# Performance work log

Hardware: AMD Instinct MI355X
Metric: run time of the kernel (lower is better)

Reference implementation:

```python
import jax, jax.numpy as jnp
import numpy as np
from jax import lax

STRIDE = (1, 1)
PADDING = ((1, 1), (1, 1))


@jax.custom_vjp
def ternary_quantize(w):
    """Quantize OIHW weights to {-1,0,+1} with per-output-channel scale alpha."""
    abs_w = jnp.abs(w)
    delta = 0.7 * abs_w.mean(axis=(1, 2, 3), keepdims=True)          # [O,1,1,1]
    ternary = jnp.where(w > delta, 1.0, jnp.where(w < -delta, -1.0, 0.0)).astype(w.dtype)
    mask = ternary != 0
    count = jnp.maximum(mask.sum(axis=(1, 2, 3), keepdims=True), 1).astype(w.dtype)
    alpha = (abs_w * mask.astype(w.dtype)).sum(axis=(1, 2, 3), keepdims=True) / count
    return ternary, alpha


def _tq_fwd(w):
    return ternary_quantize(w), w


def _tq_bwd(w, grads):
    g_ternary, _g_alpha = grads  # STE: grad_alpha is discarded
    g = jnp.where(jnp.abs(w) > 1.0, 0.0, g_ternary)
    return (g,)


ternary_quantize.defvjp(_tq_fwd, _tq_bwd)


def setup_inputs() -> dict:
    key = jax.random.key(0)
    kx, kw = jax.random.split(key)
    x = jax.random.normal(kx, (32, 256, 56, 56), dtype=jnp.float32)
    # kaiming_normal fan_out: std = sqrt(2 / (out_ch * kH * kW))
    std = np.sqrt(2.0 / (256 * 3 * 3)).astype(np.float32)
    weight = jax.random.normal(kw, (256, 256, 3, 3), dtype=jnp.float32) * std
    return {"x": x, "weight": weight}


def reference(x, weight):
    ternary, alpha = ternary_quantize(weight)
    scaled_w = alpha * ternary  # values in {-alpha_o, 0, +alpha_o}
    return lax.conv_general_dilated(
        x, scaled_w,
        window_strides=STRIDE,
        padding=PADDING,
        dimension_numbers=("NCHW", "OIHW", "NCHW"),
    )
```

## Files before the change

### kernel.cpp

```cpp
#include <hip/hip_runtime.h>
#include <hip/hip_bf16.h>

typedef unsigned short u16;
typedef __bf16 bf16x8 __attribute__((ext_vector_type(8)));
typedef float f32x4 __attribute__((ext_vector_type(4)));
typedef u16 u16x8 __attribute__((ext_vector_type(8)));

__device__ __forceinline__ u16 f2bf(float f) {
    __bf16 h = (__bf16)f;
    return __builtin_bit_cast(unsigned short, h);
}

__global__ __launch_bounds__(256) void quant_kernel(
        const float* __restrict__ w, u16* __restrict__ wq,
        float* __restrict__ alpha) {
    int o = blockIdx.x;
    int t = threadIdx.x;
    const float* wo = w + (size_t)o * 2304;
    float v[9];
    double asum = 0.0;
    #pragma unroll
    for (int i = 0; i < 9; ++i) { v[i] = wo[t * 9 + i]; asum += fabs((double)v[i]); }
    #pragma unroll
    for (int off = 32; off > 0; off >>= 1) asum += __shfl_down(asum, off, 64);
    __shared__ double red[4];
    int wv = t >> 6, lane = t & 63;
    if (lane == 0) red[wv] = asum;
    __syncthreads();
    double delta = 0.7 * ((red[0] + red[1] + red[2] + red[3]) / 2304.0);

    double msum = 0.0; int cnt = 0;
    #pragma unroll
    for (int i = 0; i < 9; ++i) {
        double f = (double)v[i];
        float tv = 0.f;
        if (f > delta) tv = 1.f;
        else if (f < -delta) tv = -1.f;
        if (tv != 0.f) { msum += fabs(f); cnt++; }
        wq[(size_t)o * 2304 + i * 256 + t] = f2bf(tv);
    }
    #pragma unroll
    for (int off = 32; off > 0; off >>= 1) {
        msum += __shfl_down(msum, off, 64);
        cnt  += __shfl_down(cnt,  off, 64);
    }
    __shared__ double red2[4];
    __shared__ int    redc[4];
    if (lane == 0) { red2[wv] = msum; redc[wv] = cnt; }
    __syncthreads();
    if (t == 0) {
        double ms = red2[0] + red2[1] + red2[2] + red2[3];
        int c = redc[0] + redc[1] + redc[2] + redc[3];
        alpha[o] = (float)(ms / (double)(c > 0 ? c : 1));
    }
}

__global__ __launch_bounds__(256) void pad_kernel(
        const float* __restrict__ x, u16* __restrict__ xp) {
    int cc  = blockIdx.x;
    int hp  = blockIdx.y;
    int img = blockIdx.z;
    int t = threadIdx.x;
    __shared__ u16 tile[64 * 57];
    bool interior = (hp >= 1) && (hp <= 56);
    if (interior) {
        int h = hp - 1;
        for (int i = t; i < 64 * 56; i += 256) {
            int c = i / 56, wcol = i - c * 56;
            float f = x[(((size_t)img * 256 + cc * 64 + c) * 56 + h) * 56 + wcol];
            tile[c * 57 + wcol] = f2bf(f);
        }
    }
    __syncthreads();
    for (int i = t; i < 58 * 64; i += 256) {
        int wl = i >> 6, c = i & 63;
        u16 val = 0;
        if (interior && wl >= 1 && wl <= 56) val = tile[c * 57 + (wl - 1)];
        xp[(((size_t)img * 58 + hp) * 58 + wl) * 256 + cc * 64 + c] = val;
    }
}

#define LDK 40

__global__ __launch_bounds__(256) void conv_gemm(
        const u16* __restrict__ Wq, const u16* __restrict__ Xp,
        const float* __restrict__ alpha, float* __restrict__ out) {
    __shared__ u16 lsA[128 * LDK];
    __shared__ u16 lsB[128 * LDK];

    int bid = blockIdx.x;
    int mt = bid & 1;
    unsigned nt = bid >> 1;
    int o_base = mt * 128;
    unsigned sp_base = nt * 128u;

    int t = threadIdx.x;
    int lane = t & 63, wave = t >> 6;
    int wm = (wave >> 1) * 64, wn = (wave & 1) * 64;

    int r = t >> 2, sub = t & 3;
    const u16* aptr0 = Wq + (size_t)(o_base + r) * 2304 + sub * 8;
    const u16* aptr1 = aptr0 + (size_t)64 * 2304;

    unsigned sp0 = sp_base + (unsigned)r;
    unsigned sp1 = sp0 + 64u;
    unsigned img0 = sp0 / 3136u, rem0 = sp0 - img0 * 3136u;
    unsigned oh0 = rem0 / 56u,   ow0 = rem0 - oh0 * 56u;
    unsigned img1 = sp1 / 3136u, rem1 = sp1 - img1 * 3136u;
    unsigned oh1 = rem1 / 56u,   ow1 = rem1 - oh1 * 56u;
    const u16* bptr0 = Xp + ((size_t)(img0 * 58 + oh0) * 58 + ow0) * 256 + sub * 8;
    const u16* bptr1 = Xp + ((size_t)(img1 * 58 + oh1) * 58 + ow1) * 256 + sub * 8;

    f32x4 acc[4][4] = {};
    u16x8 ra0, ra1, rb0, rb1;

    ra0 = *(const u16x8*)(aptr0);
    ra1 = *(const u16x8*)(aptr1);
    rb0 = *(const u16x8*)(bptr0);
    rb1 = *(const u16x8*)(bptr1);

    int row = lane & 15, quad = lane >> 4;
    int wA = r * LDK + sub * 8;
    int wA2 = (r + 64) * LDK + sub * 8;

    for (int kc = 0; kc < 72; ++kc) {
        if (kc) __syncthreads();
        *(u16x8*)&lsA[wA]  = ra0;
        *(u16x8*)&lsA[wA2] = ra1;
        *(u16x8*)&lsB[wA]  = rb0;
        *(u16x8*)&lsB[wA2] = rb1;
        __syncthreads();

        int kn = kc + 1;
        if (kn < 72) {
            int f  = kn >> 3;
            int c0 = (kn & 7) << 5;
            int kh = f / 3, kw = f - kh * 3;
            int aoff = kn * 32;
            int boff = (kh * 58 + kw) * 256 + c0;
            ra0 = *(const u16x8*)(aptr0 + aoff);
            ra1 = *(const u16x8*)(aptr1 + aoff);
            rb0 = *(const u16x8*)(bptr0 + boff);
            rb1 = *(const u16x8*)(bptr1 + boff);
        }

        bf16x8 af[4], bfr[4];
        #pragma unroll
        for (int i = 0; i < 4; ++i)
            af[i] = *(const bf16x8*)&lsA[(wm + i * 16 + row) * LDK + quad * 8];
        #pragma unroll
        for (int j = 0; j < 4; ++j)
            bfr[j] = *(const bf16x8*)&lsB[(wn + j * 16 + row) * LDK + quad * 8];
        #pragma unroll
        for (int i = 0; i < 4; ++i)
            #pragma unroll
            for (int j = 0; j < 4; ++j)
                acc[i][j] = __builtin_amdgcn_mfma_f32_16x16x32_bf16(
                                af[i], bfr[j], acc[i][j], 0, 0, 0);
    }

    int col = lane & 15;
    float al[4][4];
    #pragma unroll
    for (int i = 0; i < 4; ++i)
        #pragma unroll
        for (int rg = 0; rg < 4; ++rg)
            al[i][rg] = alpha[o_base + wm + i * 16 + quad * 4 + rg];

    #pragma unroll
    for (int j = 0; j < 4; ++j) {
        unsigned sp = sp_base + (unsigned)(wn + j * 16 + col);
        unsigned img = sp / 3136u;
        unsigned spi = sp - img * 3136u;
        float* ob = out + (size_t)img * 256 * 3136 + spi;
        #pragma unroll
        for (int i = 0; i < 4; ++i) {
            int o = o_base + wm + i * 16 + quad * 4;
            #pragma unroll
            for (int rg = 0; rg < 4; ++rg)
                ob[(size_t)(o + rg) * 3136] = acc[i][j][rg] * al[i][rg];
        }
    }
}

extern "C" void kernel_launch(void* const* d_in, const int* in_sizes, int n_in,
                              void* d_out, int out_size, void* d_ws, size_t ws_size,
                              hipStream_t stream) {
    const float* x = (const float*)d_in[0];
    const float* w = (const float*)d_in[1];
    float* out = (float*)d_out;

    char* ws = (char*)d_ws;
    u16*   xp    = (u16*)ws;
    u16*   wq    = (u16*)(ws + 55115776);
    float* alpha = (float*)(ws + 55115776 + 1179648);

    quant_kernel<<<256, 256, 0, stream>>>(w, wq, alpha);
    dim3 pg(4, 58, 32);
    pad_kernel<<<pg, 256, 0, stream>>>(x, xp);
    conv_gemm<<<784 * 2, 256, 0, stream>>>(wq, xp, alpha, out);
}
```

Before: 377.8 us.

## Use direct global-to-LDS loads with double buffering and channel-blocked input layout

Reorganizes the padded input into a channel-blocked layout of 8 channels per plane, so each wave can issue 16-byte global_load_lds transfers straight into LDS without staging through registers. The GEMM loop becomes double-buffered with one barrier per K step, and blocks are remapped so each XCD works on a contiguous range of spatial tiles for L2 locality. The pad kernel now reads with vectorized loads and writes only the interior, relying on a new full-buffer memset for the zero border. That memset adds an extra write pass over the roughly 55 MB padded buffer.

```diff
diff --git a/kernel.cpp b/kernel.cpp
--- a/kernel.cpp
+++ b/kernel.cpp
@@ -9,6 +9,12 @@
 __device__ __forceinline__ u16 f2bf(float f) {
     __bf16 h = (__bf16)f;
     return __builtin_bit_cast(unsigned short, h);
+}
+
+__device__ __forceinline__ void gl_lds16(const u16* g, u16* l) {
+    __builtin_amdgcn_global_load_lds(
+        (const __attribute__((address_space(1))) void*)g,
+        (__attribute__((address_space(3))) void*)l, 16, 0, 0);
 }
 
 __global__ __launch_bounds__(256) void quant_kernel(
@@ -57,40 +63,51 @@
 
 __global__ __launch_bounds__(256) void pad_kernel(
         const float* __restrict__ x, u16* __restrict__ xp) {
-    int cc  = blockIdx.x;
-    int hp  = blockIdx.y;
-    int img = blockIdx.z;
+    int img  = blockIdx.x;
+    int cihi = blockIdx.y;
+    int hg   = blockIdx.z;
     int t = threadIdx.x;
-    __shared__ u16 tile[64 * 57];
-    bool interior = (hp >= 1) && (hp <= 56);
-    if (interior) {
-        int h = hp - 1;
-        for (int i = t; i < 64 * 56; i += 256) {
-            int c = i / 56, wcol = i - c * 56;
-            float f = x[(((size_t)img * 256 + cc * 64 + c) * 56 + h) * 56 + wcol];
-            tile[c * 57 + wcol] = f2bf(f);
+    __shared__ u16 tile[14 * 8 * 56];
+
+    const float* xb = x + ((size_t)img * 256 + cihi * 8) * 3136 + hg * 784;
+    #pragma unroll
+    for (int k = 0; k < 7; ++k) {
+        int g = k * 256 + t;
+        if (g < 1568) {
+            int cilo = g / 196;
+            int r = g - cilo * 196;
+            f32x4 v = *(const f32x4*)(xb + (size_t)cilo * 3136 + r * 4);
+            int h = r / 14, s = r - h * 14;
+            u16* dst = &tile[(h * 8 + cilo) * 56 + s * 4];
+            dst[0] = f2bf(v[0]); dst[1] = f2bf(v[1]);
+            dst[2] = f2bf(v[2]); dst[3] = f2bf(v[3]);
         }
     }
     __syncthreads();
-    for (int i = t; i < 58 * 64; i += 256) {
-        int wl = i >> 6, c = i & 63;
-        u16 val = 0;
-        if (interior && wl >= 1 && wl <= 56) val = tile[c * 57 + (wl - 1)];
-        xp[(((size_t)img * 58 + hp) * 58 + wl) * 256 + cc * 64 + c] = val;
-    }
-}
-
-#define LDK 40
+    u16* ob = xp + (((size_t)(img * 32 + cihi) * 58 + (hg * 14 + 1)) * 58 + 1) * 8;
+    #pragma unroll
+    for (int k = 0; k < 4; ++k) {
+        int g = k * 256 + t;
+        if (g < 784) {
+            int h = g / 56, w = g - h * 56;
+            u16x8 v;
+            #pragma unroll
+            for (int j = 0; j < 8; ++j) v[j] = tile[(h * 8 + j) * 56 + w];
+            *(u16x8*)(ob + ((size_t)h * 58 + w) * 8) = v;
+        }
+    }
+}
 
 __global__ __launch_bounds__(256) void conv_gemm(
         const u16* __restrict__ Wq, const u16* __restrict__ Xp,
         const float* __restrict__ alpha, float* __restrict__ out) {
-    __shared__ u16 lsA[128 * LDK];
-    __shared__ u16 lsB[128 * LDK];
+    __shared__ u16 lsA[2][4096];
+    __shared__ u16 lsB[2][4096];
 
     int bid = blockIdx.x;
-    int mt = bid & 1;
-    unsigned nt = bid >> 1;
+    int xcd = bid & 7, idx = bid >> 3;
+    int mt = idx & 1;
+    unsigned nt = (unsigned)(xcd * 98 + (idx >> 1));
     int o_base = mt * 128;
     unsigned sp_base = nt * 128u;
 
@@ -98,65 +115,60 @@
     int lane = t & 63, wave = t >> 6;
     int wm = (wave >> 1) * 64, wn = (wave & 1) * 64;
 
-    int r = t >> 2, sub = t & 3;
-    const u16* aptr0 = Wq + (size_t)(o_base + r) * 2304 + sub * 8;
-    const u16* aptr1 = aptr0 + (size_t)64 * 2304;
-
-    unsigned sp0 = sp_base + (unsigned)r;
+    const u16* aBase0 = Wq + (size_t)(o_base + lane) * 2304;
+    const u16* aBase1 = aBase0 + (size_t)64 * 2304;
+
+    unsigned sp0 = sp_base + (unsigned)lane;
     unsigned sp1 = sp0 + 64u;
     unsigned img0 = sp0 / 3136u, rem0 = sp0 - img0 * 3136u;
     unsigned oh0 = rem0 / 56u,   ow0 = rem0 - oh0 * 56u;
     unsigned img1 = sp1 / 3136u, rem1 = sp1 - img1 * 3136u;
     unsigned oh1 = rem1 / 56u,   ow1 = rem1 - oh1 * 56u;
-    const u16* bptr0 = Xp + ((size_t)(img0 * 58 + oh0) * 58 + ow0) * 256 + sub * 8;
-    const u16* bptr1 = Xp + ((size_t)(img1 * 58 + oh1) * 58 + ow1) * 256 + sub * 8;
+    const u16* bBase0 = Xp + ((size_t)(img0 * 32) * 58 + oh0) * 58 * 8 + ow0 * 8;
+    const u16* bBase1 = Xp + ((size_t)(img1 * 32) * 58 + oh1) * 58 * 8 + ow1 * 8;
+
+    u16* dA = &lsA[0][wave * 1024];
+    u16* dB = &lsB[0][wave * 1024];
+
+    auto stage = [&](int kc, int b) {
+        int f  = kc >> 3;
+        int kh = f / 3, kw = f - kh * 3;
+        unsigned cihi = (unsigned)((kc & 7) * 4 + wave);
+        unsigned bOff = cihi * 26912u + (unsigned)kh * 464u + (unsigned)kw * 8u;
+        unsigned aOff = (unsigned)(kc * 32 + wave * 8);
+        u16* da = dA + b * 4096;
+        u16* db = dB + b * 4096;
+        gl_lds16(aBase0 + aOff, da);
+        gl_lds16(aBase1 + aOff, da + 512);
+        gl_lds16(bBase0 + bOff, db);
+        gl_lds16(bBase1 + bOff, db + 512);
+    };
 
     f32x4 acc[4][4] = {};
-    u16x8 ra0, ra1, rb0, rb1;
-
-    ra0 = *(const u16x8*)(aptr0);
-    ra1 = *(const u16x8*)(aptr1);
-    rb0 = *(const u16x8*)(bptr0);
-    rb1 = *(const u16x8*)(bptr1);
-
-    int row = lane & 15, quad = lane >> 4;
-    int wA = r * LDK + sub * 8;
-    int wA2 = (r + 64) * LDK + sub * 8;
-
+    int row16 = lane & 15, quad = lane >> 4;
+
+    stage(0, 0);
+    int p = 0;
     for (int kc = 0; kc < 72; ++kc) {
-        if (kc) __syncthreads();
-        *(u16x8*)&lsA[wA]  = ra0;
-        *(u16x8*)&lsA[wA2] = ra1;
-        *(u16x8*)&lsB[wA]  = rb0;
-        *(u16x8*)&lsB[wA2] = rb1;
         __syncthreads();
-
-        int kn = kc + 1;
-        if (kn < 72) {
-            int f  = kn >> 3;
-            int c0 = (kn & 7) << 5;
-            int kh = f / 3, kw = f - kh * 3;
-            int aoff = kn * 32;
-            int boff = (kh * 58 + kw) * 256 + c0;
-            ra0 = *(const u16x8*)(aptr0 + aoff);
-            ra1 = *(const u16x8*)(aptr1 + aoff);
-            rb0 = *(const u16x8*)(bptr0 + boff);
-            rb1 = *(const u16x8*)(bptr1 + boff);
-        }
-
+        if (kc + 1 < 72) stage(kc + 1, p ^ 1);
+
+        const u16* A = &lsA[p][0];
+        const u16* B = &lsB[p][0];
         bf16x8 af[4], bfr[4];
         #pragma unroll
         for (int i = 0; i < 4; ++i)
-            af[i] = *(const bf16x8*)&lsA[(wm + i * 16 + row) * LDK + quad * 8];
+            af[i] = *(const bf16x8*)&A[(quad * 128 + wm + i * 16 + row16) * 8];
         #pragma unroll
         for (int j = 0; j < 4; ++j)
-            bfr[j] = *(const bf16x8*)&lsB[(wn + j * 16 + row) * LDK + quad * 8];
+            bfr[j] = *(const bf16x8*)&B[(quad * 128 + wn + j * 16 + row16) * 8];
         #pragma unroll
         for (int i = 0; i < 4; ++i)
             #pragma unroll
             for (int j = 0; j < 4; ++j)
                 acc[i][j] = __builtin_amdgcn_mfma_f32_16x16x32_bf16(
                                 af[i], bfr[j], acc[i][j], 0, 0, 0);
+        p ^= 1;
     }
 
     int col = lane & 15;
@@ -196,7 +208,8 @@
     float* alpha = (float*)(ws + 55115776 + 1179648);
 
     quant_kernel<<<256, 256, 0, stream>>>(w, wq, alpha);
-    dim3 pg(4, 58, 32);
+    hipMemsetAsync(xp, 0, 55115776, stream);
+    dim3 pg(32, 32, 4);
     pad_kernel<<<pg, 256, 0, stream>>>(x, xp);
     conv_gemm<<<784 * 2, 256, 0, stream>>>(wq, xp, alpha, out);
 }
```

Result: slower. 396.9 us (+5.0%).
